# Optimization experiments

Measured on AMD Instinct MI355X. Metric: run time of the kernel, lower is better.

Reference implementation:

```python
import jax, jax.numpy as jnp
import numpy as np

B, T, D = 8, 1, 4096
H_Q, H_KV, DH = 32, 8, 128
S = 8192
K_KEEP = 128
N_REP = H_Q // H_KV


def setup_inputs() -> dict:
    key = jax.random.key(0)
    ks = jax.random.split(key, 6)
    return {
        "hidden_states": jax.random.normal(ks[0], (B, T, D), jnp.float32),
        "attn_w": jax.random.uniform(ks[1], (B, H_Q, T, S), jnp.float32),
        "k": jax.random.normal(ks[2], (B, H_KV, S, DH), jnp.float32),
        "v": jax.random.normal(ks[3], (B, H_KV, S, DH), jnp.float32),
        "Wq": jax.random.normal(ks[4], (D, D), jnp.float32) * 0.02,
        "Wo": jax.random.normal(ks[5], (D, D), jnp.float32) * 0.02,
    }


def reference(hidden_states, attn_w, k, v, Wq, Wo):
    # importance of each cached token: mean attention over heads and queries
    importance = attn_w.mean(axis=(1, 2))                      # [B, S]
    _, topk_idx = jax.lax.top_k(importance, K_KEEP)            # [B, K]
    # gather pruned KV (per-batch token selection, shared across kv heads)
    gather = jax.vmap(lambda x, idx: x[:, idx, :])             # [H_kv,S,Dh],[K] -> [H_kv,K,Dh]
    k_new = gather(k, topk_idx)                                # [B, H_kv, K, Dh]
    v_new = gather(v, topk_idx)
    # recompute attention on the pruned set
    q = (hidden_states @ Wq.T).reshape(B, T, H_Q, DH).transpose(0, 2, 1, 3)  # [B,Hq,T,Dh]
    k_all = jnp.repeat(k_new, N_REP, axis=1)                   # repeat_kv -> [B,Hq,K,Dh]
    v_all = jnp.repeat(v_new, N_REP, axis=1)
    scores = jnp.einsum('bhtd,bhsd->bhts', q, k_all) / jnp.sqrt(jnp.float32(DH))
    probs = jax.nn.softmax(scores, axis=-1)                    # [B,Hq,T,K]
    ctx = jnp.einsum('bhts,bhsd->bhtd', probs, v_all)
    ctx = ctx.transpose(0, 2, 1, 3).reshape(B, T, H_Q * DH)
    out = ctx @ Wo.T                                           # [B,T,D]
    return out, probs
```

## Files before the change

kernel.cpp:

```cpp
#include <hip/hip_runtime.h>

#define S_TOK 8192
#define NB 8
#define HQ 32
#define HKV 8
#define DH 128
#define KK 128
#define DIM 4096

__global__ __launch_bounds__(256) void importance_kernel(const float* __restrict__ attn_w,
                                                         float* __restrict__ imp) {
    int i = blockIdx.x * 256 + threadIdx.x;
    if (i >= NB * S_TOK) return;
    int b = i >> 13;
    int s = i & (S_TOK - 1);
    const float* p = attn_w + (size_t)b * HQ * S_TOK + s;
    float acc = 0.f;
#pragma unroll
    for (int h = 0; h < HQ; ++h) acc += p[(size_t)h * S_TOK];
    imp[i] = acc * (1.0f / 32.0f);
}

__global__ __launch_bounds__(256) void topk_gemvq_kernel(const float* __restrict__ imp,
                                                         int* __restrict__ topk,
                                                         const float* __restrict__ Wq,
                                                         const float* __restrict__ hidden,
                                                         float* __restrict__ q) {
    __shared__ __align__(16) unsigned mb[S_TOK];
    __shared__ __align__(16) int hist[256];
    __shared__ unsigned sprefix;
    __shared__ int skrem;
    __shared__ int nsel;
    __shared__ unsigned selb[KK];
    __shared__ int seli[KK];
    __shared__ float redg[4][NB];

    const int t = threadIdx.x;

    if (blockIdx.x >= NB) {
        const int row = blockIdx.x - NB;
        const float4* wr = (const float4*)(Wq + (size_t)row * DIM);
        float acc[NB];
#pragma unroll
        for (int b = 0; b < NB; ++b) acc[b] = 0.f;
        for (int c = t; c < DIM / 4; c += 256) {
            float4 w = wr[c];
#pragma unroll
            for (int b = 0; b < NB; ++b) {
                float4 xv = ((const float4*)(hidden + (size_t)b * DIM))[c];
                acc[b] += w.x * xv.x + w.y * xv.y + w.z * xv.z + w.w * xv.w;
            }
        }
        const int lane = t & 63, wv = t >> 6;
#pragma unroll
        for (int b = 0; b < NB; ++b) {
            float vsum = acc[b];
            for (int o = 32; o > 0; o >>= 1) vsum += __shfl_down(vsum, o);
            if (lane == 0) redg[wv][b] = vsum;
        }
        __syncthreads();
        if (t < NB) q[(size_t)t * DIM + row] = redg[0][t] + redg[1][t] + redg[2][t] + redg[3][t];
        return;
    }

    const int b = blockIdx.x;
    const float* ip = imp + (size_t)b * S_TOK;
    for (int i = t; i < S_TOK; i += 256) {
        unsigned u = __float_as_uint(ip[i]);
        u = (u & 0x80000000u) ? ~u : (u | 0x80000000u);
        mb[i] = u;
    }
    if (t == 0) { sprefix = 0u; skrem = KK; nsel = 0; }
    __syncthreads();

    for (int shift = 24; shift >= 0; shift -= 8) {
        hist[t] = 0;
        __syncthreads();
        const unsigned pfx = sprefix;
        const int krem = skrem;
        if (shift == 24) {
            for (int i = t; i < S_TOK; i += 256) {
                int bin = mb[i] >> 24;
                unsigned long long rem = __ballot(1);
                while (rem) {
                    int fl = (int)__builtin_ctzll(rem);
                    int fbin = __shfl(bin, fl);
                    unsigned long long match = __ballot(bin == fbin);
                    if ((t & 63) == fl) atomicAdd(&hist[fbin], (int)__popcll(match));
                    rem &= ~match;
                }
            }
        } else {
            const unsigned pmask = 0xFFFFFFFFu << (shift + 8);
            for (int i = t; i < S_TOK; i += 256) {
                unsigned u = mb[i];
                if ((u & pmask) == pfx) atomicAdd(&hist[(u >> shift) & 255], 1);
            }
        }
        __syncthreads();
        if (t < 64) {
            int4 h4 = *(const int4*)&hist[252 - 4 * t];
            int h0 = h4.w, h1 = h4.z, h2 = h4.y, h3 = h4.x;
            int c0 = h0, c1 = c0 + h1, c2 = c1 + h2, c3 = c2 + h3;
            int inc = c3;
#pragma unroll
            for (int o = 1; o < 64; o <<= 1) {
                int y = __shfl_up(inc, o);
                if (t >= o) inc += y;
            }
            int excl = inc - c3;
            int cand = -1, before = 0;
            if      (excl + c0 >= krem) { cand = 0; before = excl; }
            else if (excl + c1 >= krem) { cand = 1; before = excl + c0; }
            else if (excl + c2 >= krem) { cand = 2; before = excl + c1; }
            else if (excl + c3 >= krem) { cand = 3; before = excl + c2; }
            unsigned long long ball = __ballot(cand >= 0);
            int win = (int)__builtin_ctzll(ball);
            if (t == win) {
                int p = 4 * t + cand;
                sprefix = pfx | ((unsigned)(255 - p) << shift);
                skrem = krem - before;
            }
        }
        __syncthreads();
    }
    const unsigned T = sprefix;

    for (int i = t; i < S_TOK; i += 256) {
        unsigned u = mb[i];
        if (u > T) {
            int p = atomicAdd(&nsel, 1);
            selb[p] = u; seli[p] = i;
        }
    }
    __syncthreads();
    const int g = nsel;
    const int r = KK - g;

    if (t < 64) {
        int found = 0;
        for (int base0 = 0; base0 < S_TOK && found < r; base0 += 64) {
            bool is_tie = (mb[base0 + t] == T);
            unsigned long long ball = __ballot(is_tie);
            int pos = (int)__popcll(ball & ((1ull << t) - 1ull));
            if (is_tie && found + pos < r) {
                selb[g + found + pos] = T;
                seli[g + found + pos] = base0 + t;
            }
            found += (int)__popcll(ball);
        }
    }
    __syncthreads();

    for (int ksz = 2; ksz <= KK; ksz <<= 1) {
        for (int j = ksz >> 1; j > 0; j >>= 1) {
            if (t < KK) {
                int i = t, l = i ^ j;
                if (l > i) {
                    bool up = ((i & ksz) == 0);
                    unsigned ab = selb[i], cb = selb[l];
                    int ai = seli[i], ci = seli[l];
                    bool aFirst = (ab > cb) || (ab == cb && ai < ci);
                    if (up ? !aFirst : aFirst) {
                        selb[i] = cb; selb[l] = ab;
                        seli[i] = ci; seli[l] = ai;
                    }
                }
            }
            __syncthreads();
        }
    }
    if (t < KK) topk[b * KK + t] = seli[t];
}

__global__ __launch_bounds__(256) void attn_kernel(const float* __restrict__ q,
                                                   const float* __restrict__ k,
                                                   const float* __restrict__ v,
                                                   const int* __restrict__ topk,
                                                   float* __restrict__ ctx,
                                                   float* __restrict__ probs_out) {
    const int bh = blockIdx.x;
    const int b = bh >> 5, h = bh & 31, kvh = h >> 2;
    const int t = threadIdx.x;

    __shared__ float qs[DH];
    __shared__ float scs[KK];
    __shared__ float ps[KK];
    __shared__ int idxs[KK];
    __shared__ float red2[2];
    __shared__ float red3[2];
    __shared__ float ctxpart[DH];

    if (t < DH) qs[t] = q[(size_t)(b * HQ + h) * DH + t] * 0.088388347648318447f;
    if (t < KK) idxs[t] = topk[b * KK + t];
    __syncthreads();

    {
        const int tok = t >> 1, half = t & 1;
        const float4* k4 = (const float4*)(k + ((size_t)(b * HKV + kvh) * S_TOK + idxs[tok]) * DH + half * 64);
        float sc = 0.f;
#pragma unroll
        for (int d4 = 0; d4 < 16; ++d4) {
            float4 kv = k4[d4];
            int d0 = half * 64 + d4 * 4;
            sc += qs[d0] * kv.x + qs[d0 + 1] * kv.y + qs[d0 + 2] * kv.z + qs[d0 + 3] * kv.w;
        }
        sc += __shfl_xor(sc, 1);
        if (half == 0) scs[tok] = sc;
    }
    __syncthreads();

    float sc = (t < KK) ? scs[t] : -3.4e38f;
    float m = sc;
    for (int o = 32; o > 0; o >>= 1) m = fmaxf(m, __shfl_down(m, o));
    if (t < KK && (t & 63) == 0) red2[t >> 6] = m;
    __syncthreads();
    const float mx = fmaxf(red2[0], red2[1]);
    float p = (t < KK) ? expf(sc - mx) : 0.f;
    float sm = p;
    for (int o = 32; o > 0; o >>= 1) sm += __shfl_down(sm, o);
    if (t < KK && (t & 63) == 0) red3[t >> 6] = sm;
    __syncthreads();
    const float tot = red3[0] + red3[1];
    if (t < KK) {
        p /= tot;
        ps[t] = p;
        probs_out[(size_t)(b * HQ + h) * KK + t] = p;
    }
    __syncthreads();

    {
        const int d = t & (DH - 1), grp = t >> 7;
        const float* vbase = v + (size_t)(b * HKV + kvh) * S_TOK * DH;
        float acc = 0.f;
        const int s0 = grp * 64;
#pragma unroll 4
        for (int s2 = s0; s2 < s0 + 64; ++s2) {
            acc += ps[s2] * vbase[(size_t)idxs[s2] * DH + d];
        }
        if (grp == 1) ctxpart[d] = acc;
        __syncthreads();
        if (grp == 0) ctx[(size_t)(b * HQ + h) * DH + d] = acc + ctxpart[d];
    }
}

__global__ __launch_bounds__(256) void gemv_b8(const float* __restrict__ W,
                                               const float* __restrict__ x,
                                               float* __restrict__ y) {
    const int row = blockIdx.x;
    const int t = threadIdx.x;
    const float4* wr = (const float4*)(W + (size_t)row * DIM);
    float acc[NB];
#pragma unroll
    for (int b = 0; b < NB; ++b) acc[b] = 0.f;
    for (int c = t; c < DIM / 4; c += 256) {
        float4 w = wr[c];
#pragma unroll
        for (int b = 0; b < NB; ++b) {
            float4 xv = ((const float4*)(x + (size_t)b * DIM))[c];
            acc[b] += w.x * xv.x + w.y * xv.y + w.z * xv.z + w.w * xv.w;
        }
    }
    __shared__ float red[4][NB];
    const int lane = t & 63, wv = t >> 6;
#pragma unroll
    for (int b = 0; b < NB; ++b) {
        float vsum = acc[b];
        for (int o = 32; o > 0; o >>= 1) vsum += __shfl_down(vsum, o);
        if (lane == 0) red[wv][b] = vsum;
    }
    __syncthreads();
    if (t < NB) {
        y[(size_t)t * DIM + row] = red[0][t] + red[1][t] + red[2][t] + red[3][t];
    }
}

extern "C" void kernel_launch(void* const* d_in, const int* in_sizes, int n_in,
                              void* d_out, int out_size, void* d_ws, size_t ws_size,
                              hipStream_t stream) {
    const float* hidden = (const float*)d_in[0];
    const float* attn_w = (const float*)d_in[1];
    const float* k      = (const float*)d_in[2];
    const float* v      = (const float*)d_in[3];
    const float* Wq     = (const float*)d_in[4];
    const float* Wo     = (const float*)d_in[5];

    float* out   = (float*)d_out;
    float* probs = out + NB * DIM;

    char* ws = (char*)d_ws;
    float* imp  = (float*)ws;
    int*   topk = (int*)(ws + 262144);
    float* q    = (float*)(ws + 266240);
    float* ctx  = (float*)(ws + 397312);

    importance_kernel<<<(NB * S_TOK) / 256, 256, 0, stream>>>(attn_w, imp);
    topk_gemvq_kernel<<<NB + DIM, 256, 0, stream>>>(imp, topk, Wq, hidden, q);
    attn_kernel<<<NB * HQ, 256, 0, stream>>>(q, k, v, topk, ctx, probs);
    gemv_b8<<<DIM, 256, 0, stream>>>(Wo, ctx, out);
}
```

Before: 85.06 us.

## Fuse importance reduction into top-k, tile GEMVs, widen attention blocks

The head-mean importance computation moves into the top-k blocks, which read attn_w as float4 and write the sortable keys straight to LDS. This removes one launch and the workspace round-trip, but each of only 8 blocks now streams a full batch's attention weights. Both GEMVs now use a shared routine that computes 8 rows per block with the activation vector staged in LDS, cutting the block count from 4096 to 512. The attention kernel goes to 512 threads, splitting the QK dot and PV accumulation four ways. The fused kernel's large LDS footprint may limit occupancy for the GEMV blocks.

```diff
diff --git a/kernel.cpp b/kernel.cpp
--- a/kernel.cpp
+++ b/kernel.cpp
@@ -8,24 +8,64 @@
 #define KK 128
 #define DIM 4096
 
-__global__ __launch_bounds__(256) void importance_kernel(const float* __restrict__ attn_w,
-                                                         float* __restrict__ imp) {
-    int i = blockIdx.x * 256 + threadIdx.x;
-    if (i >= NB * S_TOK) return;
-    int b = i >> 13;
-    int s = i & (S_TOK - 1);
-    const float* p = attn_w + (size_t)b * HQ * S_TOK + s;
-    float acc = 0.f;
-#pragma unroll
-    for (int h = 0; h < HQ; ++h) acc += p[(size_t)h * S_TOK];
-    imp[i] = acc * (1.0f / 32.0f);
-}
-
-__global__ __launch_bounds__(256) void topk_gemvq_kernel(const float* __restrict__ imp,
-                                                         int* __restrict__ topk,
+__device__ __forceinline__ void gemv8(const float* __restrict__ W,
+                                      const float* __restrict__ x,
+                                      float* __restrict__ y,
+                                      int rstart, int t, float4* xs) {
+    const int rp = t >> 6;
+    const int lane = t & 63;
+    const int r0 = rstart + rp, r1 = rstart + rp + 4;
+    const float4* W4 = (const float4*)W;
+    const float4* x4 = (const float4*)x;
+    float acc0[NB], acc1[NB];
+#pragma unroll
+    for (int b = 0; b < NB; ++b) { acc0[b] = 0.f; acc1[b] = 0.f; }
+
+    for (int ck = 0; ck < 4; ++ck) {
+        __syncthreads();
+#pragma unroll
+        for (int i = 0; i < 8; ++i) {
+            int f = t + i * 256;
+            int b = f >> 8, c = f & 255;
+            xs[b * 256 + c] = x4[(size_t)b * (DIM / 4) + ck * 256 + c];
+        }
+        __syncthreads();
+#pragma unroll
+        for (int cc = 0; cc < 4; ++cc) {
+            const int c = lane + cc * 64;
+            float4 w0 = W4[(size_t)r0 * (DIM / 4) + ck * 256 + c];
+            float4 w1 = W4[(size_t)r1 * (DIM / 4) + ck * 256 + c];
+#pragma unroll
+            for (int b = 0; b < NB; ++b) {
+                float4 xv = xs[b * 256 + c];
+                acc0[b] += w0.x * xv.x + w0.y * xv.y + w0.z * xv.z + w0.w * xv.w;
+                acc1[b] += w1.x * xv.x + w1.y * xv.y + w1.z * xv.z + w1.w * xv.w;
+            }
+        }
+    }
+#pragma unroll
+    for (int b = 0; b < NB; ++b) {
+#pragma unroll
+        for (int o = 32; o > 0; o >>= 1) {
+            acc0[b] += __shfl_down(acc0[b], o);
+            acc1[b] += __shfl_down(acc1[b], o);
+        }
+    }
+    if (lane == 0) {
+#pragma unroll
+        for (int b = 0; b < NB; ++b) {
+            y[(size_t)b * DIM + r0] = acc0[b];
+            y[(size_t)b * DIM + r1] = acc1[b];
+        }
+    }
+}
+
+__global__ __launch_bounds__(256) void topk_gemvq_kernel(const float* __restrict__ attn_w,
                                                          const float* __restrict__ Wq,
                                                          const float* __restrict__ hidden,
+                                                         int* __restrict__ topk,
                                                          float* __restrict__ q) {
+    __shared__ __align__(16) float4 xs[NB * 256];
     __shared__ __align__(16) unsigned mb[S_TOK];
     __shared__ __align__(16) int hist[256];
     __shared__ unsigned sprefix;
@@ -33,42 +73,30 @@
     __shared__ int nsel;
     __shared__ unsigned selb[KK];
     __shared__ int seli[KK];
-    __shared__ float redg[4][NB];
 
     const int t = threadIdx.x;
-
-    if (blockIdx.x >= NB) {
-        const int row = blockIdx.x - NB;
-        const float4* wr = (const float4*)(Wq + (size_t)row * DIM);
-        float acc[NB];
-#pragma unroll
-        for (int b = 0; b < NB; ++b) acc[b] = 0.f;
-        for (int c = t; c < DIM / 4; c += 256) {
-            float4 w = wr[c];
-#pragma unroll
-            for (int b = 0; b < NB; ++b) {
-                float4 xv = ((const float4*)(hidden + (size_t)b * DIM))[c];
-                acc[b] += w.x * xv.x + w.y * xv.y + w.z * xv.z + w.w * xv.w;
-            }
-        }
-        const int lane = t & 63, wv = t >> 6;
-#pragma unroll
-        for (int b = 0; b < NB; ++b) {
-            float vsum = acc[b];
-            for (int o = 32; o > 0; o >>= 1) vsum += __shfl_down(vsum, o);
-            if (lane == 0) redg[wv][b] = vsum;
-        }
-        __syncthreads();
-        if (t < NB) q[(size_t)t * DIM + row] = redg[0][t] + redg[1][t] + redg[2][t] + redg[3][t];
+    const int bl = blockIdx.x;
+
+    if (bl >= NB) {
+        gemv8(Wq, hidden, q, (bl - NB) * 8, t, xs);
         return;
     }
 
-    const int b = blockIdx.x;
-    const float* ip = imp + (size_t)b * S_TOK;
-    for (int i = t; i < S_TOK; i += 256) {
-        unsigned u = __float_as_uint(ip[i]);
-        u = (u & 0x80000000u) ? ~u : (u | 0x80000000u);
-        mb[i] = u;
+    const int b = bl;
+    for (int base = t * 4; base < S_TOK; base += 1024) {
+        float4 acc = {0.f, 0.f, 0.f, 0.f};
+#pragma unroll 8
+        for (int h = 0; h < HQ; ++h) {
+            float4 w = *(const float4*)(attn_w + (size_t)(b * HQ + h) * S_TOK + base);
+            acc.x += w.x; acc.y += w.y; acc.z += w.z; acc.w += w.w;
+        }
+        float vals[4] = {acc.x, acc.y, acc.z, acc.w};
+#pragma unroll
+        for (int j = 0; j < 4; ++j) {
+            unsigned u = __float_as_uint(vals[j] * (1.0f / 32.0f));
+            u = (u & 0x80000000u) ? ~u : (u | 0x80000000u);
+            mb[base + j] = u;
+        }
     }
     if (t == 0) { sprefix = 0u; skrem = KK; nsel = 0; }
     __syncthreads();
@@ -105,8 +133,8 @@
             int inc = c3;
 #pragma unroll
             for (int o = 1; o < 64; o <<= 1) {
-                int y = __shfl_up(inc, o);
-                if (t >= o) inc += y;
+                int yv = __shfl_up(inc, o);
+                if (t >= o) inc += yv;
             }
             int excl = inc - c3;
             int cand = -1, before = 0;
@@ -173,7 +201,7 @@
     if (t < KK) topk[b * KK + t] = seli[t];
 }
 
-__global__ __launch_bounds__(256) void attn_kernel(const float* __restrict__ q,
+__global__ __launch_bounds__(512) void attn_kernel(const float* __restrict__ q,
                                                    const float* __restrict__ k,
                                                    const float* __restrict__ v,
                                                    const int* __restrict__ topk,
@@ -189,41 +217,47 @@
     __shared__ int idxs[KK];
     __shared__ float red2[2];
     __shared__ float red3[2];
-    __shared__ float ctxpart[DH];
+    __shared__ float part[3][DH];
 
     if (t < DH) qs[t] = q[(size_t)(b * HQ + h) * DH + t] * 0.088388347648318447f;
     if (t < KK) idxs[t] = topk[b * KK + t];
     __syncthreads();
 
     {
-        const int tok = t >> 1, half = t & 1;
-        const float4* k4 = (const float4*)(k + ((size_t)(b * HKV + kvh) * S_TOK + idxs[tok]) * DH + half * 64);
+        const int tok = t >> 2, qpart = t & 3;
+        const float4* k4 = (const float4*)(k +
+            ((size_t)(b * HKV + kvh) * S_TOK + idxs[tok]) * DH + qpart * 32);
         float sc = 0.f;
 #pragma unroll
-        for (int d4 = 0; d4 < 16; ++d4) {
+        for (int d4 = 0; d4 < 8; ++d4) {
             float4 kv = k4[d4];
-            int d0 = half * 64 + d4 * 4;
+            int d0 = qpart * 32 + d4 * 4;
             sc += qs[d0] * kv.x + qs[d0 + 1] * kv.y + qs[d0 + 2] * kv.z + qs[d0 + 3] * kv.w;
         }
         sc += __shfl_xor(sc, 1);
-        if (half == 0) scs[tok] = sc;
+        sc += __shfl_xor(sc, 2);
+        if (qpart == 0) scs[tok] = sc;
     }
     __syncthreads();
 
     float sc = (t < KK) ? scs[t] : -3.4e38f;
-    float m = sc;
-    for (int o = 32; o > 0; o >>= 1) m = fmaxf(m, __shfl_down(m, o));
-    if (t < KK && (t & 63) == 0) red2[t >> 6] = m;
+    if (t < KK) {
+        float m = sc;
+        for (int o = 32; o > 0; o >>= 1) m = fmaxf(m, __shfl_down(m, o));
+        if ((t & 63) == 0) red2[t >> 6] = m;
+    }
     __syncthreads();
     const float mx = fmaxf(red2[0], red2[1]);
-    float p = (t < KK) ? expf(sc - mx) : 0.f;
-    float sm = p;
-    for (int o = 32; o > 0; o >>= 1) sm += __shfl_down(sm, o);
-    if (t < KK && (t & 63) == 0) red3[t >> 6] = sm;
-    __syncthreads();
-    const float tot = red3[0] + red3[1];
+    float p = 0.f;
     if (t < KK) {
-        p /= tot;
+        p = expf(sc - mx);
+        float sm = p;
+        for (int o = 32; o > 0; o >>= 1) sm += __shfl_down(sm, o);
+        if ((t & 63) == 0) red3[t >> 6] = sm;
+    }
+    __syncthreads();
+    if (t < KK) {
+        p /= (red3[0] + red3[1]);
         ps[t] = p;
         probs_out[(size_t)(b * HQ + h) * KK + t] = p;
     }
@@ -233,46 +267,23 @@
         const int d = t & (DH - 1), grp = t >> 7;
         const float* vbase = v + (size_t)(b * HKV + kvh) * S_TOK * DH;
         float acc = 0.f;
-        const int s0 = grp * 64;
+        const int s0 = grp * 32;
 #pragma unroll 4
-        for (int s2 = s0; s2 < s0 + 64; ++s2) {
+        for (int s2 = s0; s2 < s0 + 32; ++s2) {
             acc += ps[s2] * vbase[(size_t)idxs[s2] * DH + d];
         }
-        if (grp == 1) ctxpart[d] = acc;
-        __syncthreads();
-        if (grp == 0) ctx[(size_t)(b * HQ + h) * DH + d] = acc + ctxpart[d];
-    }
-}
-
-__global__ __launch_bounds__(256) void gemv_b8(const float* __restrict__ W,
-                                               const float* __restrict__ x,
-                                               float* __restrict__ y) {
-    const int row = blockIdx.x;
-    const int t = threadIdx.x;
-    const float4* wr = (const float4*)(W + (size_t)row * DIM);
-    float acc[NB];
-#pragma unroll
-    for (int b = 0; b < NB; ++b) acc[b] = 0.f;
-    for (int c = t; c < DIM / 4; c += 256) {
-        float4 w = wr[c];
-#pragma unroll
-        for (int b = 0; b < NB; ++b) {
-            float4 xv = ((const float4*)(x + (size_t)b * DIM))[c];
-            acc[b] += w.x * xv.x + w.y * xv.y + w.z * xv.z + w.w * xv.w;
-        }
-    }
-    __shared__ float red[4][NB];
-    const int lane = t & 63, wv = t >> 6;
-#pragma unroll
-    for (int b = 0; b < NB; ++b) {
-        float vsum = acc[b];
-        for (int o = 32; o > 0; o >>= 1) vsum += __shfl_down(vsum, o);
-        if (lane == 0) red[wv][b] = vsum;
-    }
-    __syncthreads();
-    if (t < NB) {
-        y[(size_t)t * DIM + row] = red[0][t] + red[1][t] + red[2][t] + red[3][t];
-    }
+        if (grp) part[grp - 1][d] = acc;
+        __syncthreads();
+        if (grp == 0)
+            ctx[(size_t)(b * HQ + h) * DH + d] = acc + part[0][d] + part[1][d] + part[2][d];
+    }
+}
+
+__global__ __launch_bounds__(256) void gemv_wo_kernel(const float* __restrict__ Wo,
+                                                      const float* __restrict__ ctx,
+                                                      float* __restrict__ out) {
+    __shared__ __align__(16) float4 xs[NB * 256];
+    gemv8(Wo, ctx, out, blockIdx.x * 8, threadIdx.x, xs);
 }
 
 extern "C" void kernel_launch(void* const* d_in, const int* in_sizes, int n_in,
@@ -289,13 +300,11 @@
     float* probs = out + NB * DIM;
 
     char* ws = (char*)d_ws;
-    float* imp  = (float*)ws;
-    int*   topk = (int*)(ws + 262144);
-    float* q    = (float*)(ws + 266240);
-    float* ctx  = (float*)(ws + 397312);
-
-    importance_kernel<<<(NB * S_TOK) / 256, 256, 0, stream>>>(attn_w, imp);
-    topk_gemvq_kernel<<<NB + DIM, 256, 0, stream>>>(imp, topk, Wq, hidden, q);
-    attn_kernel<<<NB * HQ, 256, 0, stream>>>(q, k, v, topk, ctx, probs);
-    gemv_b8<<<DIM, 256, 0, stream>>>(Wo, ctx, out);
-}
+    int*   topkb = (int*)ws;
+    float* q     = (float*)(ws + 4096);
+    float* ctx   = (float*)(ws + 4096 + 131072);
+
+    topk_gemvq_kernel<<<NB + 512, 256, 0, stream>>>(attn_w, Wq, hidden, topkb, q);
+    attn_kernel<<<NB * HQ, 512, 0, stream>>>(q, k, v, topkb, ctx, probs);
+    gemv_wo_kernel<<<512, 256, 0, stream>>>(Wo, ctx, out);
+}
```

Measured after the change: 88.46 us. 4.0% more time.
